# Performance work log

Hardware: AMD Instinct MI355X
Metric: run time of the kernel (lower is better)

## Reference

```python
import jax, jax.numpy as jnp
import numpy as np
import math

B, TQ, TK, D = 4, 1024, 1024, 1024
H, DK, DV = 16, 64, 64


def _ln(x, g, b, eps=1e-5):
    m = x.mean(-1, keepdims=True)
    v = ((x - m) ** 2).mean(-1, keepdims=True)
    return (x - m) * jax.lax.rsqrt(v + eps) * g + b


def setup_inputs() -> dict:
    key = jax.random.key(0)
    ks = jax.random.split(key, 24)
    s = 0.02
    inp = {
        "x": jax.random.normal(ks[0], (B, TQ, D), jnp.float32),
        "y": jax.random.normal(ks[1], (B, TK, D), jnp.float32),
        "mask": jax.random.randint(ks[2], (B, TK), 0, 2).astype(bool),
        # pre-attention layernorms (affine)
        "ln1_g": jnp.ones((D,)), "ln1_b": jnp.zeros((D,)),
        "ln2_g": jnp.ones((D,)), "ln2_b": jnp.zeros((D,)),
        # mha1 projections
        "q_w": jax.random.normal(ks[3], (D, H * DK)) * s, "q_b": jnp.zeros((H * DK,)),
        "k_w": jax.random.normal(ks[4], (D, H * DK)) * s, "k_b": jnp.zeros((H * DK,)),
        "v_w": jax.random.normal(ks[5], (D, H * DV)) * s, "v_b": jnp.zeros((H * DV,)),
        "o_w": jax.random.normal(ks[6], (H * DV, D)) * s, "o_b": jnp.zeros((D,)),
        # MLP: [LN, ReLU, Linear] x 2 over sizes [D, D, D]
        "mln1_g": jnp.ones((D,)), "mln1_b": jnp.zeros((D,)),
        "l1_w": jax.random.normal(ks[7], (D, D)) * s, "l1_b": jnp.zeros((D,)),
        "mln2_g": jnp.ones((D,)), "mln2_b": jnp.zeros((D,)),
        "l2_w": jax.random.normal(ks[8], (D, D)) * s, "l2_b": jnp.zeros((D,)),
    }
    return inp


def reference(x, y, mask, ln1_g, ln1_b, ln2_g, ln2_b,
              q_w, q_b, k_w, k_b, v_w, v_b, o_w, o_b,
              mln1_g, mln1_b, l1_w, l1_b, mln2_g, mln2_b, l2_w, l2_b):
    # pre-norm + relu
    x1 = jax.nn.relu(_ln(x, ln1_g, ln1_b))
    y1 = jax.nn.relu(_ln(y, ln2_g, ln2_b))
    # cross attention (mha1)
    b, t, _ = x1.shape
    q = (x1 @ q_w + q_b).reshape(b, t, H, DK)
    k = (y1 @ k_w + k_b).reshape(b, -1, H, DK)
    v = (y1 @ v_w + v_b).reshape(b, -1, H, DV)
    logits = jnp.einsum('bthd,bThd->bhtT', q, k) * (1.0 / math.sqrt(DK))
    logits = jnp.where(mask[:, None, None, :], logits, -1e30)
    w = jax.nn.softmax(logits, axis=-1)
    attn = jnp.einsum('bhtT,bThd->bthd', w, v).reshape(b, t, H * DV)
    x = x + (attn @ o_w + o_b)
    # MLP: LN -> ReLU -> Linear, twice
    h = jax.nn.relu(_ln(x, mln1_g, mln1_b)) @ l1_w + l1_b
    out = jax.nn.relu(_ln(h, mln2_g, mln2_b)) @ l2_w + l2_b
    return out
```

## Files before the change

### kernel.cpp

```cpp
#include <hip/hip_runtime.h>
#include <hip/hip_bf16.h>
#include <math.h>

#define D_MODEL 1024
#define NTOK    4096

typedef unsigned short u16;
typedef unsigned int   u32;
typedef __attribute__((ext_vector_type(8))) short  short8;
typedef __attribute__((ext_vector_type(4))) float  floatx4;
typedef __attribute__((ext_vector_type(4))) unsigned short ushort4v;
typedef __attribute__((ext_vector_type(2))) unsigned int   uint2v;

static __host__ __device__ __forceinline__ float bf2f(u16 u) {
    union { unsigned int i; float f; } v; v.i = ((unsigned int)u) << 16; return v.f;
}
static __host__ __device__ __forceinline__ u16 f2bf(float f) {
    union { float f; unsigned int i; } v; v.f = f;
    unsigned int r = (v.i + 0x7FFFu + ((v.i >> 16) & 1u)) >> 16;
    return (u16)r;
}
static __device__ __forceinline__ u32 fbits(float f) {
    union { float f; u32 i; } v; v.f = f; return v.i;
}
static __device__ __forceinline__ float fexp2(float x) {
    float r; asm("v_exp_f32 %0, %1" : "=v"(r) : "v"(x)); return r;
}
static __device__ __forceinline__ void gl2lds16(const void* g, void* l) {
    __builtin_amdgcn_global_load_lds(
        (const __attribute__((address_space(1))) void*)g,
        (__attribute__((address_space(3))) void*)l, 16, 0, 0);
}
static __device__ __forceinline__ u32 lds_addr(const void* p) {
    return (u32)(size_t)(const __attribute__((address_space(3))) void*)p;
}
static __device__ __forceinline__ short8 dsr128(u32 a) {
    short8 r;
    asm volatile("ds_read_b128 %0, %1" : "=v"(r) : "v"(a));
    return r;
}

__global__ __launch_bounds__(256) void CrossTransformer_27522150432886_kernel(
    float* __restrict__ out, int n, float val)
{
    int i = blockIdx.x * 256 + threadIdx.x;
    if (i < n) out[i] = val;
}

struct PreArgs {
    const float* w[6]; u16* wt;
    const float* x; const float* g1; const float* b1; u16* xn;
    const float* y; const float* g2; const float* b2; u16* yn;
    const void* maskp; float* madd;
};
__global__ __launch_bounds__(256) void pre_k(PreArgs a)
{
    __shared__ __align__(16) char shm[2176];
    const int blk = blockIdx.x, t = threadIdx.x;

    if (blk < 6144) {
        u16 (*tile)[33] = (u16(*)[33])shm;
        const int wz = blk >> 10, tl = blk & 1023;
        const int c0 = (tl & 31) * 32, r0 = (tl >> 5) * 32;
        const int tx = t & 31, ty = t >> 5;
        const float* W  = a.w[wz];
        u16*         Wt = a.wt + (size_t)wz * D_MODEL * D_MODEL;
#pragma unroll
        for (int j = 0; j < 4; j++)
            tile[ty + j * 8][tx] = f2bf(W[(size_t)(r0 + ty + j * 8) * D_MODEL + c0 + tx]);
        __syncthreads();
#pragma unroll
        for (int j = 0; j < 4; j++)
            Wt[(size_t)(c0 + ty + j * 8) * D_MODEL + r0 + tx] = tile[tx][ty + j * 8];
        return;
    }
    if (blk < 14336) {
        const int isY = blk >= 10240;
        const int row = blk - (isY ? 10240 : 6144);
        const float* in  = isY ? a.y  : a.x;
        const float* gam = isY ? a.g2 : a.g1;
        const float* bet = isY ? a.b2 : a.b1;
        u16*         out = isY ? a.yn : a.xn;
        float (*red)[4] = (float(*)[4])shm;

        const float4 p = *(const float4*)(in + (size_t)row * D_MODEL + t * 4);
        float v0 = p.x, v1 = p.y, v2 = p.z, v3 = p.w;
        float s = v0 + v1 + v2 + v3;
        float q = v0 * v0 + v1 * v1 + v2 * v2 + v3 * v3;
#pragma unroll
        for (int off = 32; off > 0; off >>= 1) {
            s += __shfl_xor(s, off, 64);
            q += __shfl_xor(q, off, 64);
        }
        if ((t & 63) == 0) { red[0][t >> 6] = s; red[1][t >> 6] = q; }
        __syncthreads();
        s = red[0][0] + red[0][1] + red[0][2] + red[0][3];
        q = red[1][0] + red[1][1] + red[1][2] + red[1][3];
        const float mean = s * (1.0f / D_MODEL);
        const float var  = q * (1.0f / D_MODEL) - mean * mean;
        const float rstd = rsqrtf(var + 1e-5f);
        const float4 gp = *(const float4*)(gam + t * 4);
        const float4 bp = *(const float4*)(bet + t * 4);
        ushort4v o;
        o[0] = f2bf(fmaxf((v0 - mean) * rstd * gp.x + bp.x, 0.f));
        o[1] = f2bf(fmaxf((v1 - mean) * rstd * gp.y + bp.y, 0.f));
        o[2] = f2bf(fmaxf((v2 - mean) * rstd * gp.z + bp.z, 0.f));
        o[3] = f2bf(fmaxf((v3 - mean) * rstd * gp.w + bp.w, 0.f));
        *(ushort4v*)(out + (size_t)row * D_MODEL + t * 4) = o;
        return;
    }
    {
        int* rb = (int*)shm;
        const unsigned int* wv = (const unsigned int*)a.maskp;
        int bad = 0;
        for (int i = t; i < 1024; i += 256) {
            unsigned int v = wv[i];
            if (!(v == 0u || v == 1u || v == 0xFFu || v == 0xFFFFFFFFu)) bad++;
        }
#pragma unroll
        for (int off = 32; off > 0; off >>= 1) bad += __shfl_xor(bad, off, 64);
        if ((t & 63) == 0) rb[t >> 6] = bad;
        __syncthreads();
        const int Bc = rb[0] + rb[1] + rb[2] + rb[3];
        if (Bc * 2 > 1024) {
            const unsigned char* b8 = (const unsigned char*)a.maskp;
            for (int i = t; i < 4096; i += 256) a.madd[i] = b8[i] ? 0.f : -1e30f;
        } else {
            const int* m32 = (const int*)a.maskp;
            for (int i = t; i < 4096; i += 256) a.madd[i] = m32[i] ? 0.f : -1e30f;
        }
    }
}

__global__ __launch_bounds__(256) void ln_relu_k(
    const void* __restrict__ in, const float* __restrict__ gam,
    const float* __restrict__ bet, u16* __restrict__ out)
{
    const int row = blockIdx.x, t = threadIdx.x;
    ushort4v u = *(const ushort4v*)((const u16*)in + (size_t)row * D_MODEL + t * 4);
    float v0 = bf2f(u[0]), v1 = bf2f(u[1]), v2 = bf2f(u[2]), v3 = bf2f(u[3]);
    float s = v0 + v1 + v2 + v3;
    float q = v0 * v0 + v1 * v1 + v2 * v2 + v3 * v3;
#pragma unroll
    for (int off = 32; off > 0; off >>= 1) {
        s += __shfl_xor(s, off, 64);
        q += __shfl_xor(q, off, 64);
    }
    __shared__ float red[2][4];
    if ((t & 63) == 0) { red[0][t >> 6] = s; red[1][t >> 6] = q; }
    __syncthreads();
    s = red[0][0] + red[0][1] + red[0][2] + red[0][3];
    q = red[1][0] + red[1][1] + red[1][2] + red[1][3];

    const float mean = s * (1.0f / D_MODEL);
    const float var  = q * (1.0f / D_MODEL) - mean * mean;
    const float rstd = rsqrtf(var + 1e-5f);

    const float4 gp = *(const float4*)(gam + t * 4);
    const float4 bp = *(const float4*)(bet + t * 4);
    ushort4v o;
    o[0] = f2bf(fmaxf((v0 - mean) * rstd * gp.x + bp.x, 0.f));
    o[1] = f2bf(fmaxf((v1 - mean) * rstd * gp.y + bp.y, 0.f));
    o[2] = f2bf(fmaxf((v2 - mean) * rstd * gp.z + bp.z, 0.f));
    o[3] = f2bf(fmaxf((v3 - mean) * rstd * gp.w + bp.w, 0.f));
    *(ushort4v*)(out + (size_t)row * D_MODEL + t * 4) = o;
}

struct GB {
    const u16* A; const u16* Bt; const float* bias; const float* resid;
    u16* C; float* Cf; float scale; int vt;
};
struct GB3 { GB g[3]; u16* VtG; };

__global__ __launch_bounds__(512) void gemm_qkv256_k(GB3 gb)
{
    extern __shared__ char smc[];
    const int lin = blockIdx.x;
    const int t8  = (lin & 7) * 24 + (lin >> 3);
    const int z   = t8 >> 6;
    const int rem = t8 & 63;
    const GB cfg = gb.g[z];
    const int t = threadIdx.x, lane = t & 63, w = t >> 6;
    const int wy = w >> 2, wx = w & 3;
    const int bm = (rem >> 2) * 256, bn = (rem & 3) * 256;
    const int m = lane & 15, g = lane >> 4;
    const int srcseg = ((t & 3) ^ ((t >> 3) & 3)) * 8;
    const int gsw    = (g ^ ((m >> 1) & 3)) * 8;

    const u16* Ag = cfg.A  + (size_t)(bm + (t >> 2)) * D_MODEL + srcseg;
    const u16* Bg = cfg.Bt + (size_t)(bn + (t >> 2)) * D_MODEL + srcseg;

    auto stage_half = [&](int kt, int s, int buf) {
        const int koff = kt + s * 32;
        char* base = smc + buf * 65536 + s * 32768;
        gl2lds16(Ag + koff,                 base + t * 16);
        gl2lds16(Ag + 128 * D_MODEL + koff, base + 8192 + t * 16);
        gl2lds16(Bg + koff,                 base + 16384 + t * 16);
        gl2lds16(Bg + 128 * D_MODEL + koff, base + 24576 + t * 16);
    };

    const u32 smb  = lds_addr(smc);
    const u32 offA = smb + (u32)(((wy * 128 + m) * 32 + gsw) * 2);
    const u32 offB = smb + 16384u + (u32)(((wx * 64 + m) * 32 + gsw) * 2);

    floatx4 acc[8][4] = {};
    const int NT = D_MODEL / 64;

    stage_half(0, 0, 0);
    stage_half(0, 1, 0);

    int buf = 0;
    for (int tt = 0; tt < NT; ++tt) {
        const int ktn = ((tt + 1) & (NT - 1)) * 64;
        const int nbuf = buf ^ 1;
#pragma unroll
        for (int s = 0; s < 2; ++s) {
            asm volatile("s_waitcnt vmcnt(4)" ::: "memory");
            __builtin_amdgcn_s_barrier();
            __builtin_amdgcn_sched_barrier(0);
            stage_half(ktn, s, nbuf);

            const u32 reg = (u32)(buf * 65536 + s * 32768);
            short8 af[8], bf[4];
#pragma unroll
            for (int mt = 0; mt < 8; mt++)
                af[mt] = dsr128(offA + reg + mt * 1024);
#pragma unroll
            for (int nt = 0; nt < 4; nt++)
                bf[nt] = dsr128(offB + reg + nt * 1024);
            asm volatile("s_waitcnt lgkmcnt(0)");
            __builtin_amdgcn_sched_barrier(0);

            __builtin_amdgcn_s_setprio(1);
#pragma unroll
            for (int mt = 0; mt < 8; mt++)
#pragma unroll
                for (int nt = 0; nt < 4; nt++)
                    acc[mt][nt] = __builtin_amdgcn_mfma_f32_16x16x32_bf16(
                        af[mt], bf[nt], acc[mt][nt], 0, 0, 0);
            __builtin_amdgcn_s_setprio(0);
        }
        buf ^= 1;
    }
    asm volatile("s_waitcnt vmcnt(0)" ::: "memory");
    __builtin_amdgcn_s_barrier();

    float bv[4];
#pragma unroll
    for (int nt = 0; nt < 4; nt++)
        bv[nt] = cfg.bias[bn + wx * 64 + nt * 16 + m];

    if (!cfg.vt) {
#pragma unroll
        for (int mt = 0; mt < 8; mt++)
#pragma unroll
            for (int r = 0; r < 4; r++) {
                const int grow = bm + wy * 128 + mt * 16 + g * 4 + r;
#pragma unroll
                for (int nt = 0; nt < 4; nt++) {
                    const int col = bn + wx * 64 + nt * 16 + m;
                    float val = (acc[mt][nt][r] + bv[nt]) * cfg.scale;
                    cfg.C[(size_t)grow * D_MODEL + col] = f2bf(val);
                }
            }
    } else {
        const int b    = bm >> 10;
        const int tok0 = bm & 1023;
#pragma unroll
        for (int mt = 0; mt < 8; mt++) {
            const int tok = tok0 + wy * 128 + mt * 16 + g * 4;
#pragma unroll
            for (int nt = 0; nt < 4; nt++) {
                const int col = bn + wx * 64 + nt * 16 + m;
                const int h = col >> 6, d = col & 63;
                ushort4v o;
                o[0] = f2bf(acc[mt][nt][0] + bv[nt]);
                o[1] = f2bf(acc[mt][nt][1] + bv[nt]);
                o[2] = f2bf(acc[mt][nt][2] + bv[nt]);
                o[3] = f2bf(acc[mt][nt][3] + bv[nt]);
                *(ushort4v*)(gb.VtG + ((size_t)((b * 16 + h) * 64 + d)) * 1024 + tok) = o;
            }
        }
    }
}

__global__ __launch_bounds__(512) void gemm_out_k(GB cfg)
{
    const int lin = blockIdx.x + 8 * blockIdx.y;
    const int t8  = (lin & 7) * 32 + (lin >> 3);
    __shared__ __align__(16) u16 sm[3 * 8192];
    const int t = threadIdx.x, lane = t & 63, w = t >> 6;
    const int wy = w >> 2, wx = w & 3;
    const int bm = (t8 >> 3) * 128, bn = (t8 & 7) * 128;
    const int m = lane & 15, g = lane >> 4;
    const int arow = t >> 2;
    const int aseg = ((t & 3) ^ ((t >> 3) & 3)) * 8;
    const int gsw  = (g ^ ((m >> 1) & 3)) * 8;

    const u16* Ag = cfg.A  + (size_t)(bm + arow) * D_MODEL + aseg;
    const u16* Bg = cfg.Bt + (size_t)(bn + arow) * D_MODEL + aseg;

    auto stage = [&](int k0, int s) {
        char* dst = (char*)sm + s * 16384;
        gl2lds16(Ag + k0, dst + w * 1024);
        gl2lds16(Bg + k0, dst + 8192 + w * 1024);
    };

    const u32 smb  = lds_addr(sm);
    const u32 offA = smb + (u32)(((wy * 64 + m) * 32 + gsw) * 2);
    const u32 offB = smb + 8192u + (u32)(((wx * 32 + m) * 32 + gsw) * 2);

    floatx4 acc[4][2] = {};
    const int NT = D_MODEL / 32;

    stage(0, 0);
    stage(32, 1);
    asm volatile("s_waitcnt vmcnt(2)" ::: "memory");
    __builtin_amdgcn_s_barrier();
    __builtin_amdgcn_sched_barrier(0);

    int sb = 0;
    for (int tt = 0; tt < NT; ++tt) {
        int tp = tt + 2; if (tp >= NT) tp -= NT;
        int sbp = sb + 2; if (sbp >= 3) sbp -= 3;
        stage(tp * 32, sbp);

        const u32 reg = (u32)(sb * 16384);
        short8 af[4], bf[2];
#pragma unroll
        for (int mt = 0; mt < 4; mt++)
            af[mt] = dsr128(offA + reg + mt * 1024);
#pragma unroll
        for (int nt = 0; nt < 2; nt++)
            bf[nt] = dsr128(offB + reg + nt * 1024);
        asm volatile("s_waitcnt lgkmcnt(0)");
        __builtin_amdgcn_sched_barrier(0);

        __builtin_amdgcn_s_setprio(1);
#pragma unroll
        for (int mt = 0; mt < 4; mt++)
#pragma unroll
            for (int nt = 0; nt < 2; nt++)
                acc[mt][nt] = __builtin_amdgcn_mfma_f32_16x16x32_bf16(
                    af[mt], bf[nt], acc[mt][nt], 0, 0, 0);
        __builtin_amdgcn_s_setprio(0);

        asm volatile("s_waitcnt vmcnt(2)" ::: "memory");
        __builtin_amdgcn_s_barrier();
        __builtin_amdgcn_sched_barrier(0);
        sb = sb + 1; if (sb >= 3) sb -= 3;
    }
    asm volatile("s_waitcnt vmcnt(0)" ::: "memory");

    float bv[2]; int cols[2];
#pragma unroll
    for (int nt = 0; nt < 2; nt++) {
        cols[nt] = bn + wx * 32 + nt * 16 + m;
        bv[nt]   = cfg.bias[cols[nt]];
    }
#pragma unroll
    for (int mt = 0; mt < 4; mt++) {
#pragma unroll
        for (int r = 0; r < 4; r++) {
            const int grow = bm + wy * 64 + mt * 16 + g * 4 + r;
#pragma unroll
            for (int nt = 0; nt < 2; nt++) {
                float val = acc[mt][nt][r] + bv[nt];
                if (cfg.resid) val += cfg.resid[(size_t)grow * D_MODEL + cols[nt]];
                if (cfg.Cf) cfg.Cf[(size_t)grow * D_MODEL + cols[nt]] = val;
                else        cfg.C [(size_t)grow * D_MODEL + cols[nt]] = f2bf(val);
            }
        }
    }
}

__global__ __launch_bounds__(256) void attn_k(
    const u16* __restrict__ Q, const u16* __restrict__ Kk,
    const u16* __restrict__ VtG, const float* __restrict__ maddG,
    u16* __restrict__ Ob)
{
    __shared__ __align__(16) char smraw[55808];
    u16*   KsB  = (u16*)smraw;
    u16*   VtB  = (u16*)(smraw + 16384);
    u16*   Ps   = (u16*)(smraw + 32768);
    float* madd = (float*)(smraw + 51200);
    float* liS  = (float*)(smraw + 55296);

    const int lin = blockIdx.x + 8 * (blockIdx.y + 16 * blockIdx.z);
    const int tw  = (lin & 7) * 64 + (lin >> 3);
    const int qt = tw & 7, h = (tw >> 3) & 15, b = tw >> 7;
    const int t = threadIdx.x, lane = t & 63, w = t >> 6;
    const int m = lane & 15, g = lane >> 4;

    for (int i = t; i < 1024; i += 256) madd[i] = maddG[b * 1024 + i];

    short8 qf[2][2];
    const u16* Qb = Q + ((size_t)(b * 1024 + qt * 128 + w * 32 + m)) * D_MODEL + h * 64 + g * 8;
#pragma unroll
    for (int q2 = 0; q2 < 2; q2++)
#pragma unroll
        for (int hf = 0; hf < 2; hf++)
            qf[q2][hf] = *(const short8*)(Qb + q2 * 16 * D_MODEL + hf * 32);

    u16* Pw = Ps + w * 32 * 72;
    const u16* Kp = Kk  + (size_t)(b * 1024) * D_MODEL + h * 64;
    const u16* Vp = VtG + (size_t)((b * 16 + h) * 64) * 1024;

    const int r0 = lane >> 3;
    const int ssl = ((lane & 7) ^ r0) * 8;
    auto stageKV = [&](int kt, int bufI) {
#pragma unroll
        for (int i = 0; i < 2; i++) {
            const int row = w * 16 + i * 8 + r0;
            gl2lds16(Kp + (size_t)(kt + row) * D_MODEL + ssl,
                     (char*)(KsB + bufI * 4096) + (w * 2 + i) * 1024);
            gl2lds16(Vp + (size_t)row * 1024 + kt + ssl,
                     (char*)(VtB + bufI * 4096) + (w * 2 + i) * 1024);
        }
    };

    floatx4 Ov[2][4] = {};
    float li[2] = { 0.f, 0.f };

    const int s8  = m & 7;
    const int sl0 = (g ^ s8) * 8;
    const int sl1 = sl0 ^ 32;

    stageKV(0, 0);
    __syncthreads();

    int buf = 0;
    for (int kt = 0; kt < 1024; kt += 64) {
        if (kt + 64 < 1024) stageKV(kt + 64, buf ^ 1);

        const u16* Ks = KsB + buf * 4096;
        const u16* Vt = VtB + buf * 4096;

        short8 af[4][2];
        float4 md[4];
#pragma unroll
        for (int tile = 0; tile < 4; tile++) {
            af[tile][0] = *(const short8*)(Ks + (tile * 16 + m) * 64 + sl0);
            af[tile][1] = *(const short8*)(Ks + (tile * 16 + m) * 64 + sl1);
            md[tile]    = *(const float4*)(madd + kt + tile * 16 + g * 4);
        }

#pragma unroll
        for (int q2 = 0; q2 < 2; q2++) {
            floatx4 st[4];
            __builtin_amdgcn_s_setprio(1);
#pragma unroll
            for (int tile = 0; tile < 4; tile++) {
                floatx4 z = {};
                z = __builtin_amdgcn_mfma_f32_16x16x32_bf16(af[tile][0], qf[q2][0], z, 0, 0, 0);
                st[tile] = __builtin_amdgcn_mfma_f32_16x16x32_bf16(af[tile][1], qf[q2][1], z, 0, 0, 0);
            }
            __builtin_amdgcn_s_setprio(0);
            float rs = 0.f;
#pragma unroll
            for (int tile = 0; tile < 4; tile++) {
                float p0 = fexp2(st[tile][0] + md[tile].x);
                float p1 = fexp2(st[tile][1] + md[tile].y);
                float p2 = fexp2(st[tile][2] + md[tile].z);
                float p3 = fexp2(st[tile][3] + md[tile].w);
                rs += (p0 + p1) + (p2 + p3);
                uint2v pk;
                pk[0] = __builtin_amdgcn_perm(fbits(p1), fbits(p0), 0x07060302u);
                pk[1] = __builtin_amdgcn_perm(fbits(p3), fbits(p2), 0x07060302u);
                *(uint2v*)(Pw + (q2 * 16 + m) * 72 + tile * 16 + g * 4) = pk;
            }
            rs += __shfl_xor(rs, 16, 64);
            rs += __shfl_xor(rs, 32, 64);
            li[q2] += rs;
        }

        short8 pa[2][2], vb[4][2];
#pragma unroll
        for (int q2 = 0; q2 < 2; q2++) {
            pa[q2][0] = *(const short8*)(Pw + (q2 * 16 + m) * 72 + g * 8);
            pa[q2][1] = *(const short8*)(Pw + (q2 * 16 + m) * 72 + 32 + g * 8);
        }
#pragma unroll
        for (int nt = 0; nt < 4; nt++) {
            vb[nt][0] = *(const short8*)(Vt + (nt * 16 + m) * 64 + sl0);
            vb[nt][1] = *(const short8*)(Vt + (nt * 16 + m) * 64 + sl1);
        }
        __builtin_amdgcn_s_setprio(1);
#pragma unroll
        for (int q2 = 0; q2 < 2; q2++)
#pragma unroll
            for (int nt = 0; nt < 4; nt++) {
                Ov[q2][nt] = __builtin_amdgcn_mfma_f32_16x16x32_bf16(
                    pa[q2][0], vb[nt][0], Ov[q2][nt], 0, 0, 0);
                Ov[q2][nt] = __builtin_amdgcn_mfma_f32_16x16x32_bf16(
                    pa[q2][1], vb[nt][1], Ov[q2][nt], 0, 0, 0);
            }
        __builtin_amdgcn_s_setprio(0);

        asm volatile("s_waitcnt vmcnt(0)" ::: "memory");
        __builtin_amdgcn_s_barrier();
        buf ^= 1;
    }

    if (g == 0) { liS[w * 32 + m] = li[0]; liS[w * 32 + 16 + m] = li[1]; }
    __builtin_amdgcn_s_waitcnt(0);
    float4 inv4[2];
#pragma unroll
    for (int q2 = 0; q2 < 2; q2++) {
        float4 l4 = *(const float4*)(liS + w * 32 + q2 * 16 + g * 4);
        inv4[q2].x = 1.0f / fmaxf(l4.x, 1e-37f);
        inv4[q2].y = 1.0f / fmaxf(l4.y, 1e-37f);
        inv4[q2].z = 1.0f / fmaxf(l4.z, 1e-37f);
        inv4[q2].w = 1.0f / fmaxf(l4.w, 1e-37f);
    }
#pragma unroll
    for (int q2 = 0; q2 < 2; q2++) {
        const float iv[4] = { inv4[q2].x, inv4[q2].y, inv4[q2].z, inv4[q2].w };
#pragma unroll
        for (int nt = 0; nt < 4; nt++)
#pragma unroll
            for (int r = 0; r < 4; r++) {
                const int tok = qt * 128 + w * 32 + q2 * 16 + g * 4 + r;
                Ob[(size_t)(b * 1024 + tok) * D_MODEL + h * 64 + nt * 16 + m] =
                    f2bf(Ov[q2][nt][r] * iv[r]);
            }
    }
}

extern "C" __attribute__((visibility("default")))
void kernel_launch(void* const* d_in, const int* in_sizes, int n_in,
                   void* d_out, int out_size, void* d_ws, size_t ws_size,
                   hipStream_t stream)
{
    (void)in_sizes; (void)n_in;
    const float* x      = (const float*)d_in[0];
    const float* y      = (const float*)d_in[1];
    const void*  maskp  = d_in[2];
    const float* ln1_g  = (const float*)d_in[3];
    const float* ln1_b  = (const float*)d_in[4];
    const float* ln2_g  = (const float*)d_in[5];
    const float* ln2_b  = (const float*)d_in[6];
    const float* q_w    = (const float*)d_in[7];
    const float* q_b    = (const float*)d_in[8];
    const float* k_w    = (const float*)d_in[9];
    const float* k_b    = (const float*)d_in[10];
    const float* v_w    = (const float*)d_in[11];
    const float* v_b    = (const float*)d_in[12];
    const float* o_w    = (const float*)d_in[13];
    const float* o_b    = (const float*)d_in[14];
    const float* mln1_g = (const float*)d_in[15];
    const float* mln1_b = (const float*)d_in[16];
    const float* l1_w   = (const float*)d_in[17];
    const float* l1_b   = (const float*)d_in[18];
    const float* mln2_g = (const float*)d_in[19];
    const float* mln2_b = (const float*)d_in[20];
    const float* l2_w   = (const float*)d_in[21];
    const float* l2_b   = (const float*)d_in[22];

    const int nout = out_size;
    const size_t MB = 1024 * 1024;
    if (ws_size < 61 * MB) {
        CrossTransformer_27522150432886_kernel<<<(nout + 255) / 256, 256, 0, stream>>>(
            (float*)d_out, nout, 7.0f);
        return;
    }

    static bool attrSet = false;
    if (!attrSet) {
        hipFuncSetAttribute((const void*)gemm_qkv256_k,
                            hipFuncAttributeMaxDynamicSharedMemorySize, 131072);
        attrSet = true;
    }

    char* ws = (char*)d_ws;
    const size_t WE = (size_t)D_MODEL * D_MODEL;
    u16*   wt   = (u16*)(ws);
    u16*   xn   = (u16*)(ws + 12 * MB);
    u16*   yn   = (u16*)(ws + 20 * MB);
    u16*   Qb   = (u16*)(ws + 28 * MB);
    u16*   Kb   = (u16*)(ws + 36 * MB);
    u16*   VtG  = (u16*)(ws + 44 * MB);
    u16*   attn = (u16*)(ws + 52 * MB);
    float* madd = (float*)(ws + 60 * MB);
    u16* x2 = xn; u16* m1n = Qb; u16* hb = Kb; u16* m2n = VtG;

    PreArgs pa;
    pa.w[0] = q_w; pa.w[1] = k_w; pa.w[2] = v_w;
    pa.w[3] = o_w; pa.w[4] = l1_w; pa.w[5] = l2_w;
    pa.wt = wt;
    pa.x = x; pa.g1 = ln1_g; pa.b1 = ln1_b; pa.xn = xn;
    pa.y = y; pa.g2 = ln2_g; pa.b2 = ln2_b; pa.yn = yn;
    pa.maskp = maskp; pa.madd = madd;
    pre_k<<<14337, 256, 0, stream>>>(pa);

    const float qscale = 0.18033688011112042f;
    GB3 qkv = {};
    qkv.g[0] = GB{ xn, wt + 0 * WE, q_b, nullptr, Qb, nullptr, qscale, 0 };
    qkv.g[1] = GB{ yn, wt + 1 * WE, k_b, nullptr, Kb, nullptr, 1.0f,  0 };
    qkv.g[2] = GB{ yn, wt + 2 * WE, v_b, nullptr, nullptr, nullptr, 1.0f, 1 };
    qkv.VtG = VtG;
    gemm_qkv256_k<<<192, 512, 131072, stream>>>(qkv);

    attn_k<<<dim3(8, 16, 4), 256, 0, stream>>>(Qb, Kb, VtG, madd, attn);

    GB go = GB{ attn, wt + 3 * WE, o_b, x, x2, nullptr, 1.0f, 0 };
    gemm_out_k<<<dim3(8, 32, 1), 512, 0, stream>>>(go);

    ln_relu_k<<<NTOK, 256, 0, stream>>>(x2, mln1_g, mln1_b, m1n);

    GB g1 = GB{ m1n, wt + 4 * WE, l1_b, nullptr, hb, nullptr, 1.0f, 0 };
    gemm_out_k<<<dim3(8, 32, 1), 512, 0, stream>>>(g1);

    ln_relu_k<<<NTOK, 256, 0, stream>>>(hb, mln2_g, mln2_b, m2n);

    GB g2 = GB{ m2n, wt + 5 * WE, l2_b, nullptr, nullptr, (float*)d_out, 1.0f, 0 };
    gemm_out_k<<<dim3(8, 32, 1), 512, 0, stream>>>(g2);
}
```

Before: 269.0 us.

## Fuse output projection, MLP layernorms and GEMMs into one persistent kernel with grid barriers

The five tail launches (out-proj GEMM, LN, L1 GEMM, LN, L2 GEMM) are merged into a single 256-block persistent kernel that uses atomic-counter grid barriers between phases. The barrier counters are zeroed inside the preprocessing kernel. The aim is to remove launch gaps and tail effects between small dependent kernels. In exchange it adds spin-wait barriers, depends on all 256 blocks being co-resident, and does the LN phases with fewer, larger blocks.

```diff
diff --git a/kernel.cpp b/kernel.cpp
--- a/kernel.cpp
+++ b/kernel.cpp
@@ -39,6 +39,18 @@
     asm volatile("ds_read_b128 %0, %1" : "=v"(r) : "v"(a));
     return r;
 }
+static __device__ __forceinline__ void gridbar(int* cnt, int ph) {
+    __syncthreads();
+    if (threadIdx.x == 0) {
+        __threadfence();
+        atomicAdd(&cnt[ph], 1);
+        while (__hip_atomic_load(&cnt[ph], __ATOMIC_ACQUIRE,
+                                 __HIP_MEMORY_SCOPE_AGENT) < 256)
+            __builtin_amdgcn_s_sleep(8);
+        __threadfence();
+    }
+    __syncthreads();
+}
 
 __global__ __launch_bounds__(256) void CrossTransformer_27522150432886_kernel(
     float* __restrict__ out, int n, float val)
@@ -51,7 +63,7 @@
     const float* w[6]; u16* wt;
     const float* x; const float* g1; const float* b1; u16* xn;
     const float* y; const float* g2; const float* b2; u16* yn;
-    const void* maskp; float* madd;
+    const void* maskp; float* madd; int* cnt;
 };
 __global__ __launch_bounds__(256) void pre_k(PreArgs a)
 {
@@ -110,6 +122,7 @@
         return;
     }
     {
+        if (t < 4) a.cnt[t] = 0;
         int* rb = (int*)shm;
         const unsigned int* wv = (const unsigned int*)a.maskp;
         int bad = 0;
@@ -130,40 +143,6 @@
             for (int i = t; i < 4096; i += 256) a.madd[i] = m32[i] ? 0.f : -1e30f;
         }
     }
-}
-
-__global__ __launch_bounds__(256) void ln_relu_k(
-    const void* __restrict__ in, const float* __restrict__ gam,
-    const float* __restrict__ bet, u16* __restrict__ out)
-{
-    const int row = blockIdx.x, t = threadIdx.x;
-    ushort4v u = *(const ushort4v*)((const u16*)in + (size_t)row * D_MODEL + t * 4);
-    float v0 = bf2f(u[0]), v1 = bf2f(u[1]), v2 = bf2f(u[2]), v3 = bf2f(u[3]);
-    float s = v0 + v1 + v2 + v3;
-    float q = v0 * v0 + v1 * v1 + v2 * v2 + v3 * v3;
-#pragma unroll
-    for (int off = 32; off > 0; off >>= 1) {
-        s += __shfl_xor(s, off, 64);
-        q += __shfl_xor(q, off, 64);
-    }
-    __shared__ float red[2][4];
-    if ((t & 63) == 0) { red[0][t >> 6] = s; red[1][t >> 6] = q; }
-    __syncthreads();
-    s = red[0][0] + red[0][1] + red[0][2] + red[0][3];
-    q = red[1][0] + red[1][1] + red[1][2] + red[1][3];
-
-    const float mean = s * (1.0f / D_MODEL);
-    const float var  = q * (1.0f / D_MODEL) - mean * mean;
-    const float rstd = rsqrtf(var + 1e-5f);
-
-    const float4 gp = *(const float4*)(gam + t * 4);
-    const float4 bp = *(const float4*)(bet + t * 4);
-    ushort4v o;
-    o[0] = f2bf(fmaxf((v0 - mean) * rstd * gp.x + bp.x, 0.f));
-    o[1] = f2bf(fmaxf((v1 - mean) * rstd * gp.y + bp.y, 0.f));
-    o[2] = f2bf(fmaxf((v2 - mean) * rstd * gp.z + bp.z, 0.f));
-    o[3] = f2bf(fmaxf((v3 - mean) * rstd * gp.w + bp.w, 0.f));
-    *(ushort4v*)(out + (size_t)row * D_MODEL + t * 4) = o;
 }
 
 struct GB {
@@ -284,11 +263,13 @@
     }
 }
 
-__global__ __launch_bounds__(512) void gemm_out_k(GB cfg)
-{
-    const int lin = blockIdx.x + 8 * blockIdx.y;
+static __device__ void gemm_core(
+    const u16* __restrict__ A, const u16* __restrict__ Bt,
+    const float* __restrict__ bias, const float* __restrict__ resid,
+    u16* __restrict__ C, float* __restrict__ Cf, u16* sm)
+{
+    const int lin = blockIdx.x;
     const int t8  = (lin & 7) * 32 + (lin >> 3);
-    __shared__ __align__(16) u16 sm[3 * 8192];
     const int t = threadIdx.x, lane = t & 63, w = t >> 6;
     const int wy = w >> 2, wx = w & 3;
     const int bm = (t8 >> 3) * 128, bn = (t8 & 7) * 128;
@@ -297,8 +278,8 @@
     const int aseg = ((t & 3) ^ ((t >> 3) & 3)) * 8;
     const int gsw  = (g ^ ((m >> 1) & 3)) * 8;
 
-    const u16* Ag = cfg.A  + (size_t)(bm + arow) * D_MODEL + aseg;
-    const u16* Bg = cfg.Bt + (size_t)(bn + arow) * D_MODEL + aseg;
+    const u16* Ag = A  + (size_t)(bm + arow) * D_MODEL + aseg;
+    const u16* Bg = Bt + (size_t)(bn + arow) * D_MODEL + aseg;
 
     auto stage = [&](int k0, int s) {
         char* dst = (char*)sm + s * 16384;
@@ -356,7 +337,7 @@
 #pragma unroll
     for (int nt = 0; nt < 2; nt++) {
         cols[nt] = bn + wx * 32 + nt * 16 + m;
-        bv[nt]   = cfg.bias[cols[nt]];
+        bv[nt]   = bias[cols[nt]];
     }
 #pragma unroll
     for (int mt = 0; mt < 4; mt++) {
@@ -366,12 +347,78 @@
 #pragma unroll
             for (int nt = 0; nt < 2; nt++) {
                 float val = acc[mt][nt][r] + bv[nt];
-                if (cfg.resid) val += cfg.resid[(size_t)grow * D_MODEL + cols[nt]];
-                if (cfg.Cf) cfg.Cf[(size_t)grow * D_MODEL + cols[nt]] = val;
-                else        cfg.C [(size_t)grow * D_MODEL + cols[nt]] = f2bf(val);
+                if (resid) val += resid[(size_t)grow * D_MODEL + cols[nt]];
+                if (Cf) Cf[(size_t)grow * D_MODEL + cols[nt]] = val;
+                else    C [(size_t)grow * D_MODEL + cols[nt]] = f2bf(val);
             }
         }
     }
+}
+
+static __device__ void ln_rows(const u16* __restrict__ in,
+                               const float* __restrict__ gam,
+                               const float* __restrict__ bet,
+                               u16* __restrict__ out, float* redl)
+{
+    const int t = threadIdx.x;
+    const int g2 = t >> 8, tt = t & 255;
+    const int rowbase = blockIdx.x * 16;
+#pragma unroll 1
+    for (int r = 0; r < 16; r += 2) {
+        const int row = rowbase + r + g2;
+        ushort4v u = *(const ushort4v*)(in + (size_t)row * D_MODEL + tt * 4);
+        float v0 = bf2f(u[0]), v1 = bf2f(u[1]), v2 = bf2f(u[2]), v3 = bf2f(u[3]);
+        float s = v0 + v1 + v2 + v3;
+        float q = v0 * v0 + v1 * v1 + v2 * v2 + v3 * v3;
+#pragma unroll
+        for (int off = 32; off > 0; off >>= 1) {
+            s += __shfl_xor(s, off, 64);
+            q += __shfl_xor(q, off, 64);
+        }
+        if ((tt & 63) == 0) {
+            redl[g2 * 8 + (tt >> 6)]     = s;
+            redl[g2 * 8 + 4 + (tt >> 6)] = q;
+        }
+        __syncthreads();
+        s = redl[g2 * 8 + 0] + redl[g2 * 8 + 1] + redl[g2 * 8 + 2] + redl[g2 * 8 + 3];
+        q = redl[g2 * 8 + 4] + redl[g2 * 8 + 5] + redl[g2 * 8 + 6] + redl[g2 * 8 + 7];
+        const float mean = s * (1.0f / D_MODEL);
+        const float var  = q * (1.0f / D_MODEL) - mean * mean;
+        const float rstd = rsqrtf(var + 1e-5f);
+        const float4 gp = *(const float4*)(gam + tt * 4);
+        const float4 bp = *(const float4*)(bet + tt * 4);
+        ushort4v o;
+        o[0] = f2bf(fmaxf((v0 - mean) * rstd * gp.x + bp.x, 0.f));
+        o[1] = f2bf(fmaxf((v1 - mean) * rstd * gp.y + bp.y, 0.f));
+        o[2] = f2bf(fmaxf((v2 - mean) * rstd * gp.z + bp.z, 0.f));
+        o[3] = f2bf(fmaxf((v3 - mean) * rstd * gp.w + bp.w, 0.f));
+        *(ushort4v*)(out + (size_t)row * D_MODEL + tt * 4) = o;
+        __syncthreads();
+    }
+}
+
+struct TailArgs {
+    const u16* attn; const u16* wtO; const float* o_b; const float* x;  u16* x2;
+    const float* mg1; const float* mb1; u16* m1n;
+    const u16* wt1; const float* l1_b; u16* hb;
+    const float* mg2; const float* mb2; u16* m2n;
+    const u16* wt2; const float* l2_b; float* out;
+    int* cnt;
+};
+__global__ __launch_bounds__(512) void tail_k(TailArgs a)
+{
+    __shared__ __align__(16) u16 sm[3 * 8192];
+    __shared__ float redl[16];
+
+    gemm_core(a.attn, a.wtO, a.o_b, a.x, a.x2, nullptr, sm);
+    gridbar(a.cnt, 0);
+    ln_rows(a.x2, a.mg1, a.mb1, a.m1n, redl);
+    gridbar(a.cnt, 1);
+    gemm_core(a.m1n, a.wt1, a.l1_b, nullptr, a.hb, nullptr, sm);
+    gridbar(a.cnt, 2);
+    ln_rows(a.hb, a.mg2, a.mb2, a.m2n, redl);
+    gridbar(a.cnt, 3);
+    gemm_core(a.m2n, a.wt2, a.l2_b, nullptr, nullptr, a.out, sm);
 }
 
 __global__ __launch_bounds__(256) void attn_k(
@@ -559,7 +606,7 @@
 
     const int nout = out_size;
     const size_t MB = 1024 * 1024;
-    if (ws_size < 61 * MB) {
+    if (ws_size < 63 * MB) {
         CrossTransformer_27522150432886_kernel<<<(nout + 255) / 256, 256, 0, stream>>>(
             (float*)d_out, nout, 7.0f);
         return;
@@ -582,6 +629,7 @@
     u16*   VtG  = (u16*)(ws + 44 * MB);
     u16*   attn = (u16*)(ws + 52 * MB);
     float* madd = (float*)(ws + 60 * MB);
+    int*   cnt  = (int*)(ws + 62 * MB);
     u16* x2 = xn; u16* m1n = Qb; u16* hb = Kb; u16* m2n = VtG;
 
     PreArgs pa;
@@ -590,7 +638,7 @@
     pa.wt = wt;
     pa.x = x; pa.g1 = ln1_g; pa.b1 = ln1_b; pa.xn = xn;
     pa.y = y; pa.g2 = ln2_g; pa.b2 = ln2_b; pa.yn = yn;
-    pa.maskp = maskp; pa.madd = madd;
+    pa.maskp = maskp; pa.madd = madd; pa.cnt = cnt;
     pre_k<<<14337, 256, 0, stream>>>(pa);
 
     const float qscale = 0.18033688011112042f;
@@ -603,16 +651,12 @@
 
     attn_k<<<dim3(8, 16, 4), 256, 0, stream>>>(Qb, Kb, VtG, madd, attn);
 
-    GB go = GB{ attn, wt + 3 * WE, o_b, x, x2, nullptr, 1.0f, 0 };
-    gemm_out_k<<<dim3(8, 32, 1), 512, 0, stream>>>(go);
-
-    ln_relu_k<<<NTOK, 256, 0, stream>>>(x2, mln1_g, mln1_b, m1n);
-
-    GB g1 = GB{ m1n, wt + 4 * WE, l1_b, nullptr, hb, nullptr, 1.0f, 0 };
-    gemm_out_k<<<dim3(8, 32, 1), 512, 0, stream>>>(g1);
-
-    ln_relu_k<<<NTOK, 256, 0, stream>>>(hb, mln2_g, mln2_b, m2n);
-
-    GB g2 = GB{ m2n, wt + 5 * WE, l2_b, nullptr, nullptr, (float*)d_out, 1.0f, 0 };
-    gemm_out_k<<<dim3(8, 32, 1), 512, 0, stream>>>(g2);
-}
+    TailArgs ta;
+    ta.attn = attn; ta.wtO = wt + 3 * WE; ta.o_b = o_b; ta.x = x; ta.x2 = x2;
+    ta.mg1 = mln1_g; ta.mb1 = mln1_b; ta.m1n = m1n;
+    ta.wt1 = wt + 4 * WE; ta.l1_b = l1_b; ta.hb = hb;
+    ta.mg2 = mln2_g; ta.mb2 = mln2_b; ta.m2n = m2n;
+    ta.wt2 = wt + 5 * WE; ta.l2_b = l2_b; ta.out = (float*)d_out;
+    ta.cnt = cnt;
+    tail_k<<<256, 512, 0, stream>>>(ta);
+}
```

Result: slower. 381.4 us (+41.8%).
